# Kernel optimization log

Hardware: AMD Instinct MI355X
Metric: run time of the kernel (lower is better)

## Reference

```python
import jax, jax.numpy as jnp
import numpy as np

D_MODEL = 512
N_HEADS = 8
B, S = 4, 1024
REL_HIDDEN = 64


def setup_inputs() -> dict:
    key = jax.random.key(0)
    ks = jax.random.split(key, 16)

    def g(k, shape, scale=0.02):
        return jax.random.normal(k, shape, dtype=jnp.float32) * scale

    x = jax.random.normal(ks[0], (B, S, D_MODEL), dtype=jnp.float32)
    freqs = jax.random.uniform(ks[1], (B, S, 1), dtype=jnp.float32)
    return {
        "x": x,
        "freqs": freqs,
        "Wq": g(ks[2], (D_MODEL, D_MODEL)), "bq": g(ks[3], (D_MODEL,)),
        "Wk": g(ks[4], (D_MODEL, D_MODEL)), "bk": g(ks[5], (D_MODEL,)),
        "Wv": g(ks[6], (D_MODEL, D_MODEL)), "bv": g(ks[7], (D_MODEL,)),
        "Wo": g(ks[8], (D_MODEL, D_MODEL)), "bo": g(ks[9], (D_MODEL,)),
        "W1": g(ks[10], (2, REL_HIDDEN)), "b1": g(ks[11], (REL_HIDDEN,)),
        "W2": g(ks[12], (REL_HIDDEN, N_HEADS)), "b2": g(ks[13], (N_HEADS,)),
    }


def reference(x, freqs, Wq, bq, Wk, bk, Wv, bv, Wo, bo, W1, b1, W2, b2):
    b, s, d = x.shape
    h = N_HEADS
    dh = d // h

    def proj(W, bias):  # (b,s,d) -> (b,h,s,dh)
        return (x @ W + bias).reshape(b, s, h, dh).transpose(0, 2, 1, 3)

    Q = proj(Wq, bq)
    K = proj(Wk, bk)
    V = proj(Wv, bv)

    scores = jnp.einsum('bhid,bhjd->bhij', Q, K) / jnp.sqrt(jnp.float32(dh))

    # per-pair relative-frequency features: (b,s,s,2)
    eps = 1e-6
    fd = freqs[:, :, None, :] - freqs[:, None, :, :]
    fr = jnp.log((freqs[:, :, None, :] + eps) / (freqs[:, None, :, :] + eps))
    rel = jnp.concatenate([fd, fr], axis=-1)

    # MLP bias -> (b,s,s,h) -> (b,h,s,s)
    bias = jax.nn.relu(rel @ W1 + b1) @ W2 + b2
    scores = scores + jnp.transpose(bias, (0, 3, 1, 2))

    attn = jax.nn.softmax(scores, axis=-1)
    ctx = jnp.einsum('bhij,bhjd->bhid', attn, V)
    ctx = ctx.transpose(0, 2, 1, 3).reshape(b, s, d)
    return ctx @ Wo + bo
```

## Files before the change

kernel.cpp:

```cpp
#include <hip/hip_runtime.h>
#include <hip/hip_bf16.h>
#include <cstdint>

#define BATCH   4
#define SEQ     1024
#define DM      512
#define NH      8
#define DH      64
#define RH      64

typedef float f32x4 __attribute__((ext_vector_type(4)));
typedef __bf16 bf16x8 __attribute__((ext_vector_type(8)));

#define QB_OFF    (0)
#define KB_OFF    (4  << 20)
#define VT_OFF    (8  << 20)
#define XB_OFF    (12 << 20)
#define WT_OFF    (16 << 20)
#define WOT_OFF   (18 << 20)
#define AW_OFF    (20 << 20)
#define CW_OFF    (21 << 20)
#define CTXB_OFF  (22 << 20)
#define BIAS_OFF  (32 << 20)

__global__ __launch_bounds__(256) void cast_x(
    const float* __restrict__ x, __bf16* __restrict__ xb)
{
    const size_t i = ((size_t)blockIdx.x * 256 + threadIdx.x) * 8;
    const float4 a = *(const float4*)&x[i];
    const float4 b = *(const float4*)&x[i + 4];
    bf16x8 o;
    o[0] = (__bf16)a.x; o[1] = (__bf16)a.y; o[2] = (__bf16)a.z; o[3] = (__bf16)a.w;
    o[4] = (__bf16)b.x; o[5] = (__bf16)b.y; o[6] = (__bf16)b.z; o[7] = (__bf16)b.w;
    *(bf16x8*)&xb[i] = o;
}

__global__ __launch_bounds__(256) void cast_w(
    const float* __restrict__ Wq, const float* __restrict__ Wk,
    const float* __restrict__ Wv, const float* __restrict__ Wo,
    __bf16* __restrict__ Wt, __bf16* __restrict__ Wot)
{
    const int t = threadIdx.x;
    const int k0 = blockIdx.x * 64;
    const int n0 = blockIdx.y * 64;
    const int z  = blockIdx.z;
    const float* __restrict__ src = (z == 0) ? Wq : (z == 1) ? Wk : (z == 2) ? Wv : Wo;
    __bf16* __restrict__ dst = (z < 3) ? (Wt + (size_t)(z * 512 + n0) * 512)
                                       : (Wot + (size_t)n0 * 512);

    __shared__ __align__(16) float Ts[64][65];
    #pragma unroll
    for (int i = 0; i < 4; ++i) {
        const int id = t + i * 256;
        const int row = id >> 4, c4 = (id & 15) * 4;
        const float4 v = *(const float4*)&src[(size_t)(k0 + row) * DM + n0 + c4];
        Ts[row][c4 + 0] = v.x; Ts[row][c4 + 1] = v.y;
        Ts[row][c4 + 2] = v.z; Ts[row][c4 + 3] = v.w;
    }
    __syncthreads();
    #pragma unroll
    for (int i = 0; i < 2; ++i) {
        const int id = t + i * 256;
        const int rn = id >> 3, ck = (id & 7) * 8;
        bf16x8 o;
        #pragma unroll
        for (int j = 0; j < 8; ++j) o[j] = (__bf16)Ts[ck + j][rn];
        *(bf16x8*)&dst[(size_t)rn * 512 + k0 + ck] = o;
    }
}

__global__ __launch_bounds__(256) void gemm_qkv_mfma(
    const __bf16* __restrict__ xb, const __bf16* __restrict__ Wt,
    const float* __restrict__ bq, const float* __restrict__ bk,
    const float* __restrict__ bv,
    __bf16* __restrict__ Qb, __bf16* __restrict__ Kb, __bf16* __restrict__ Vtb)
{
    const int t = threadIdx.x;
    const int wave = t >> 6, lane = t & 63;
    const int wm = wave >> 1, wn = wave & 1;
    const int r = lane & 15, kc = lane >> 4, q4 = kc * 4;
    const int m0 = blockIdx.y * 128;
    const int n0 = blockIdx.x * 128;
    const int sec = n0 >> 9;
    const int nn = n0 & 511;

    __shared__ __align__(16) char smem[36864];
    __bf16* __restrict__ As = (__bf16*)smem;
    __bf16* __restrict__ Bs = (__bf16*)(smem + 18432);

    f32x4 acc[4][4];
    #pragma unroll
    for (int i = 0; i < 4; ++i)
        #pragma unroll
        for (int j = 0; j < 4; ++j) acc[i][j] = {0.f, 0.f, 0.f, 0.f};

    const int srow = t >> 3, sck = (t & 7) * 8;
    const __bf16* __restrict__ Ag = xb + (size_t)(m0 + srow) * 512 + sck;
    const __bf16* __restrict__ Bg = Wt + (size_t)(n0 + srow) * 512 + sck;

    for (int k0 = 0; k0 < 512; k0 += 64) {
        bf16x8 ra[4], rb[4];
        #pragma unroll
        for (int i = 0; i < 4; ++i) {
            ra[i] = *(const bf16x8*)(Ag + (size_t)i * 32 * 512 + k0);
            rb[i] = *(const bf16x8*)(Bg + (size_t)i * 32 * 512 + k0);
        }
        __syncthreads();
        #pragma unroll
        for (int i = 0; i < 4; ++i) {
            *(bf16x8*)&As[(srow + i * 32) * 72 + sck] = ra[i];
            *(bf16x8*)&Bs[(srow + i * 32) * 72 + sck] = rb[i];
        }
        __syncthreads();
        #pragma unroll
        for (int ks = 0; ks < 2; ++ks) {
            bf16x8 af[4], bf[4];
            #pragma unroll
            for (int mf = 0; mf < 4; ++mf)
                af[mf] = *(const bf16x8*)&As[(wm * 64 + mf * 16 + r) * 72 + ks * 32 + kc * 8];
            #pragma unroll
            for (int nf = 0; nf < 4; ++nf)
                bf[nf] = *(const bf16x8*)&Bs[(wn * 64 + nf * 16 + r) * 72 + ks * 32 + kc * 8];
            #pragma unroll
            for (int mf = 0; mf < 4; ++mf)
                #pragma unroll
                for (int nf = 0; nf < 4; ++nf)
                    acc[mf][nf] = __builtin_amdgcn_mfma_f32_16x16x32_bf16(
                        af[mf], bf[nf], acc[mf][nf], 0, 0, 0);
        }
    }

    const float* __restrict__ bias = (sec == 0) ? bq : (sec == 1) ? bk : bv;
    __syncthreads();
    __bf16* __restrict__ Ls = (__bf16*)smem;
    if (sec < 2) {
        #pragma unroll
        for (int mf = 0; mf < 4; ++mf)
            #pragma unroll
            for (int nf = 0; nf < 4; ++nf) {
                const int n_l = wn * 64 + nf * 16 + r;
                const float bb = bias[nn + n_l];
                #pragma unroll
                for (int rr = 0; rr < 4; ++rr)
                    Ls[(wm * 64 + mf * 16 + q4 + rr) * 136 + n_l] =
                        (__bf16)(acc[mf][nf][rr] + bb);
            }
    } else {
        #pragma unroll
        for (int mf = 0; mf < 4; ++mf)
            #pragma unroll
            for (int nf = 0; nf < 4; ++nf) {
                const int n_l = wn * 64 + nf * 16 + r;
                const float bb = bias[nn + n_l];
                #pragma unroll
                for (int rr = 0; rr < 4; ++rr)
                    Ls[n_l * 136 + (wm * 64 + mf * 16 + q4 + rr)] =
                        (__bf16)(acc[mf][nf][rr] + bb);
            }
    }
    __syncthreads();

    const int b = m0 >> 10, sbase = m0 & 1023;
    if (sec < 2) {
        __bf16* __restrict__ dst = sec ? Kb : Qb;
        #pragma unroll
        for (int i = 0; i < 8; ++i) {
            const int id = t + i * 256;
            const int row = id >> 4, nc = (id & 15) * 8;
            const bf16x8 v = *(const bf16x8*)&Ls[row * 136 + nc];
            const int ng = nn + nc, h = ng >> 6, c = ng & 63;
            *(bf16x8*)&dst[((size_t)(b * NH + h) * SEQ + sbase + row) * DH + c] = v;
        }
    } else {
        #pragma unroll
        for (int i = 0; i < 8; ++i) {
            const int id = t + i * 256;
            const int nrow = id >> 4, mc = (id & 15) * 8;
            const bf16x8 v = *(const bf16x8*)&Ls[nrow * 136 + mc];
            const int ng = nn + nrow, h = ng >> 6, c = ng & 63;
            *(bf16x8*)&Vtb[((size_t)(b * NH + h) * DH + c) * SEQ + sbase + mc] = v;
        }
    }
}

__global__ __launch_bounds__(256) void gemm_out_mfma(
    const __bf16* __restrict__ ctxb, const __bf16* __restrict__ Wot,
    const float* __restrict__ bo, float* __restrict__ out)
{
    const int t = threadIdx.x;
    const int wave = t >> 6, lane = t & 63;
    const int wm = wave >> 1, wn = wave & 1;
    const int r = lane & 15, kc = lane >> 4, q4 = kc * 4;
    const int m0 = blockIdx.y * 128;
    const int n0 = blockIdx.x * 128;

    __shared__ __align__(16) char smem[36864];
    __bf16* __restrict__ As = (__bf16*)smem;
    __bf16* __restrict__ Bs = (__bf16*)(smem + 18432);

    f32x4 acc[4][4];
    #pragma unroll
    for (int i = 0; i < 4; ++i)
        #pragma unroll
        for (int j = 0; j < 4; ++j) acc[i][j] = {0.f, 0.f, 0.f, 0.f};

    const int srow = t >> 3, sck = (t & 7) * 8;
    const __bf16* __restrict__ Ag = ctxb + (size_t)(m0 + srow) * 512 + sck;
    const __bf16* __restrict__ Bg = Wot + (size_t)(n0 + srow) * 512 + sck;

    for (int k0 = 0; k0 < 512; k0 += 64) {
        bf16x8 ra[4], rb[4];
        #pragma unroll
        for (int i = 0; i < 4; ++i) {
            ra[i] = *(const bf16x8*)(Ag + (size_t)i * 32 * 512 + k0);
            rb[i] = *(const bf16x8*)(Bg + (size_t)i * 32 * 512 + k0);
        }
        __syncthreads();
        #pragma unroll
        for (int i = 0; i < 4; ++i) {
            *(bf16x8*)&As[(srow + i * 32) * 72 + sck] = ra[i];
            *(bf16x8*)&Bs[(srow + i * 32) * 72 + sck] = rb[i];
        }
        __syncthreads();
        #pragma unroll
        for (int ks = 0; ks < 2; ++ks) {
            bf16x8 af[4], bf[4];
            #pragma unroll
            for (int mf = 0; mf < 4; ++mf)
                af[mf] = *(const bf16x8*)&As[(wm * 64 + mf * 16 + r) * 72 + ks * 32 + kc * 8];
            #pragma unroll
            for (int nf = 0; nf < 4; ++nf)
                bf[nf] = *(const bf16x8*)&Bs[(wn * 64 + nf * 16 + r) * 72 + ks * 32 + kc * 8];
            #pragma unroll
            for (int mf = 0; mf < 4; ++mf)
                #pragma unroll
                for (int nf = 0; nf < 4; ++nf)
                    acc[mf][nf] = __builtin_amdgcn_mfma_f32_16x16x32_bf16(
                        af[mf], bf[nf], acc[mf][nf], 0, 0, 0);
        }
    }

    #pragma unroll
    for (int mf = 0; mf < 4; ++mf)
        #pragma unroll
        for (int nf = 0; nf < 4; ++nf) {
            const int n_l = wn * 64 + nf * 16 + r;
            const float bb = bo[n0 + n_l];
            #pragma unroll
            for (int rr = 0; rr < 4; ++rr)
                out[(size_t)(m0 + wm * 64 + mf * 16 + q4 + rr) * DM + n0 + n_l] =
                    acc[mf][nf][rr] + bb;
        }
}

__global__ __launch_bounds__(64) void rel_kernel(
    const float* __restrict__ freqs,
    const float* __restrict__ W1,
    const float* __restrict__ b1,
    float* __restrict__ Aw,
    float* __restrict__ Cw)
{
    const int row = blockIdx.x;
    const int k = threadIdx.x;
    const float f = freqs[row];
    const float L = logf(f + 1e-6f);
    const float base = f * W1[k] + L * W1[RH + k];
    Aw[(size_t)row * RH + k] = base + b1[k];
    Cw[(size_t)row * RH + k] = -base;
}

__global__ __launch_bounds__(256) void bias_kernel(
    const float* __restrict__ Aw, const float* __restrict__ Cw,
    const float* __restrict__ W2, __bf16* __restrict__ biasb)
{
    const int t = threadIdx.x;
    const int j0 = blockIdx.x * 64;
    const int i0 = blockIdx.y * 16;
    const int b  = blockIdx.z;

    __shared__ __align__(16) float Ast[64][20];
    __shared__ __align__(16) float Cs[64][68];
    __shared__ __align__(16) float W2s[64][8];

    {
        const int rr = t >> 4, kq = (t & 15) * 4;
        float4 a4 = *(const float4*)&Aw[((size_t)b * SEQ + i0 + rr) * RH + kq];
        Ast[kq + 0][rr] = a4.x;
        Ast[kq + 1][rr] = a4.y;
        Ast[kq + 2][rr] = a4.z;
        Ast[kq + 3][rr] = a4.w;
        const int jr = t >> 2, kq2 = (t & 3) * 16;
        #pragma unroll
        for (int q = 0; q < 4; ++q) {
            float4 c4 = *(const float4*)&Cw[((size_t)b * SEQ + j0 + jr) * RH + kq2 + q * 4];
            Cs[kq2 + q * 4 + 0][jr] = c4.x;
            Cs[kq2 + q * 4 + 1][jr] = c4.y;
            Cs[kq2 + q * 4 + 2][jr] = c4.z;
            Cs[kq2 + q * 4 + 3][jr] = c4.w;
        }
        if (t < 64) {
            *(float4*)&W2s[t][0] = *(const float4*)&W2[t * 8 + 0];
            *(float4*)&W2s[t][4] = *(const float4*)&W2[t * 8 + 4];
        }
    }
    __syncthreads();

    const int jl = t & 63, ig = t >> 6;
    float acc[4][8];
    #pragma unroll
    for (int ii = 0; ii < 4; ++ii)
        #pragma unroll
        for (int hh = 0; hh < 8; ++hh) acc[ii][hh] = 0.f;

    #pragma unroll 4
    for (int k = 0; k < 64; ++k) {
        const float c  = Cs[k][jl];
        const float4 a4 = *(const float4*)&Ast[k][ig * 4];
        const float4 w0 = *(const float4*)&W2s[k][0];
        const float4 w1 = *(const float4*)&W2s[k][4];
        const float hv[4] = {
            fmaxf(a4.x + c, 0.f), fmaxf(a4.y + c, 0.f),
            fmaxf(a4.z + c, 0.f), fmaxf(a4.w + c, 0.f)};
        #pragma unroll
        for (int ii = 0; ii < 4; ++ii) {
            acc[ii][0] = fmaf(hv[ii], w0.x, acc[ii][0]);
            acc[ii][1] = fmaf(hv[ii], w0.y, acc[ii][1]);
            acc[ii][2] = fmaf(hv[ii], w0.z, acc[ii][2]);
            acc[ii][3] = fmaf(hv[ii], w0.w, acc[ii][3]);
            acc[ii][4] = fmaf(hv[ii], w1.x, acc[ii][4]);
            acc[ii][5] = fmaf(hv[ii], w1.y, acc[ii][5]);
            acc[ii][6] = fmaf(hv[ii], w1.z, acc[ii][6]);
            acc[ii][7] = fmaf(hv[ii], w1.w, acc[ii][7]);
        }
    }

    #pragma unroll
    for (int hh = 0; hh < 8; ++hh)
        #pragma unroll
        for (int ii = 0; ii < 4; ++ii)
            biasb[(((size_t)b * NH + hh) * SEQ + i0 + ig * 4 + ii) * SEQ + j0 + jl]
                = (__bf16)acc[ii][hh];
}

#define SSTR 1028
#define PSTR 1032

__global__ __launch_bounds__(512) void attn_mfma(
    const __bf16* __restrict__ Qb, const __bf16* __restrict__ Kb,
    const __bf16* __restrict__ Vtb, const __bf16* __restrict__ biasb,
    __bf16* __restrict__ ctxb)
{
    const int t = threadIdx.x;
    const int wave = t >> 6, lane = t & 63;
    const int r = lane & 15, kc = lane >> 4;
    const int blk = blockIdx.x;
    const int it = blk & 63;
    const int h  = (blk >> 6) & 7;
    const int b  = blk >> 9;
    const int s0 = it * 16;
    const int bh = b * NH + h;

    __shared__ __align__(16) float Ss[16 * SSTR];
    __shared__ float invl[16];

    {
        const __bf16* __restrict__ Qp = Qb + ((size_t)bh * SEQ + s0) * DH;
        const __bf16* __restrict__ Kp = Kb + (size_t)bh * SEQ * DH;
        const bf16x8 qa0 = *(const bf16x8*)(Qp + r * DH + kc * 8);
        const bf16x8 qa1 = *(const bf16x8*)(Qp + r * DH + 32 + kc * 8);
        #pragma unroll
        for (int jt = 0; jt < 8; ++jt) {
            const int j0 = wave * 128 + jt * 16;
            const bf16x8 kb0 = *(const bf16x8*)(Kp + (size_t)(j0 + r) * DH + kc * 8);
            const bf16x8 kb1 = *(const bf16x8*)(Kp + (size_t)(j0 + r) * DH + 32 + kc * 8);
            f32x4 acc = {0.f, 0.f, 0.f, 0.f};
            acc = __builtin_amdgcn_mfma_f32_16x16x32_bf16(qa0, kb0, acc, 0, 0, 0);
            acc = __builtin_amdgcn_mfma_f32_16x16x32_bf16(qa1, kb1, acc, 0, 0, 0);
            #pragma unroll
            for (int rr = 0; rr < 4; ++rr)
                Ss[(kc * 4 + rr) * SSTR + j0 + r] = acc[rr] * 0.125f;
        }
    }
    __syncthreads();

    {
        const int row = t >> 5, ln = t & 31;
        const __bf16* __restrict__ bp =
            biasb + ((size_t)bh * SEQ + (s0 + row)) * SEQ;
        float sv[32];
        float m = -1e30f;
        #pragma unroll
        for (int jj = 0; jj < 32; ++jj) {
            const float s = Ss[row * SSTR + jj * 32 + ln] + (float)bp[jj * 32 + ln];
            sv[jj] = s;
            m = fmaxf(m, s);
        }
        #pragma unroll
        for (int mask = 16; mask >= 1; mask >>= 1)
            m = fmaxf(m, __shfl_xor(m, mask));
        float l = 0.f;
        #pragma unroll
        for (int jj = 0; jj < 32; ++jj) {
            const float p = __expf(sv[jj] - m);
            sv[jj] = p;
            l += p;
        }
        #pragma unroll
        for (int mask = 16; mask >= 1; mask >>= 1)
            l += __shfl_xor(l, mask);
        if (ln == 0) invl[row] = 1.0f / l;
        __syncthreads();
        __bf16* __restrict__ Pb = (__bf16*)Ss;
        #pragma unroll
        for (int jj = 0; jj < 32; ++jj)
            Pb[row * PSTR + jj * 32 + ln] = (__bf16)sv[jj];
    }
    __syncthreads();

    {
        const int ct = wave & 3, kh = wave >> 2;
        const __bf16* __restrict__ Pb = (const __bf16*)Ss;
        const __bf16* __restrict__ Vp =
            Vtb + ((size_t)bh * DH + ct * 16 + r) * SEQ + kh * 512;
        f32x4 acc = {0.f, 0.f, 0.f, 0.f};
        #pragma unroll 4
        for (int jt = 0; jt < 16; ++jt) {
            const bf16x8 pa = *(const bf16x8*)(Pb + (size_t)r * PSTR + kh * 512 + jt * 32 + kc * 8);
            const bf16x8 vb = *(const bf16x8*)(Vp + jt * 32 + kc * 8);
            acc = __builtin_amdgcn_mfma_f32_16x16x32_bf16(pa, vb, acc, 0, 0, 0);
        }
        float* __restrict__ part = Ss + 8256;
        if (kh == 1) {
            #pragma unroll
            for (int rr = 0; rr < 4; ++rr)
                part[ct * 272 + (kc * 4 + rr) * 17 + r] = acc[rr];
        }
        __syncthreads();
        if (kh == 0) {
            #pragma unroll
            for (int rr = 0; rr < 4; ++rr) {
                const int row = kc * 4 + rr;
                const float v = (acc[rr] + part[ct * 272 + row * 17 + r]) * invl[row];
                ctxb[((size_t)(b * SEQ) + s0 + row) * DM + h * DH + ct * 16 + r] = (__bf16)v;
            }
        }
    }
}

extern "C" void kernel_launch(void* const* d_in, const int* in_sizes, int n_in,
                              void* d_out, int out_size, void* d_ws, size_t ws_size,
                              hipStream_t stream)
{
    const float* x     = (const float*)d_in[0];
    const float* freqs = (const float*)d_in[1];
    const float* Wq    = (const float*)d_in[2];
    const float* bq    = (const float*)d_in[3];
    const float* Wk    = (const float*)d_in[4];
    const float* bk    = (const float*)d_in[5];
    const float* Wv    = (const float*)d_in[6];
    const float* bv    = (const float*)d_in[7];
    const float* Wo    = (const float*)d_in[8];
    const float* bo    = (const float*)d_in[9];
    const float* W1    = (const float*)d_in[10];
    const float* b1    = (const float*)d_in[11];
    const float* W2    = (const float*)d_in[12];

    char* wsb = (char*)d_ws;
    __bf16* Qb    = (__bf16*)(wsb + QB_OFF);
    __bf16* Kb    = (__bf16*)(wsb + KB_OFF);
    __bf16* Vtb   = (__bf16*)(wsb + VT_OFF);
    __bf16* xb    = (__bf16*)(wsb + XB_OFF);
    __bf16* Wt    = (__bf16*)(wsb + WT_OFF);
    __bf16* Wot   = (__bf16*)(wsb + WOT_OFF);
    float*  Aw    = (float*)(wsb + AW_OFF);
    float*  Cw    = (float*)(wsb + CW_OFF);
    __bf16* ctxb  = (__bf16*)(wsb + CTXB_OFF);
    __bf16* biasb = (__bf16*)(wsb + BIAS_OFF);
    float* out = (float*)d_out;

    cast_x<<<dim3(1024), 256, 0, stream>>>(x, xb);
    cast_w<<<dim3(8, 8, 4), 256, 0, stream>>>(Wq, Wk, Wv, Wo, Wt, Wot);
    gemm_qkv_mfma<<<dim3(12, 32), 256, 0, stream>>>(xb, Wt, bq, bk, bv, Qb, Kb, Vtb);
    rel_kernel<<<dim3(4096), 64, 0, stream>>>(freqs, W1, b1, Aw, Cw);
    bias_kernel<<<dim3(16, 64, 4), 256, 0, stream>>>(Aw, Cw, W2, biasb);
    attn_mfma<<<dim3(2048), 512, 0, stream>>>(Qb, Kb, Vtb, biasb, ctxb);
    gemm_out_mfma<<<dim3(4, 32), 256, 0, stream>>>(ctxb, Wot, bo, out);
}
```

Baseline: 239.8 us.

## Compute relative-position bias MLP with MFMA and vectorize attention bias loads

Replaces the scalar-FMA bias kernel with an MFMA version: the ReLU hidden activations are built per pair in bf16 and multiplied by a bf16, zero-padded transposed W2 using 16x16x32 MFMA, with larger j tiles per block. The attention kernel now prefetches its bias row with 16-byte vector loads before the QK^T stage, vectorizes the softmax reads and P stores, and raises wave priority around the MFMA loops. This targets the FP32 ALU cost of the per-pair MLP and the scattered 2-byte bias loads, at the cost of rounding hidden activations to bf16 and wasting half the MFMA output rows on padding heads.

```diff
diff --git a/kernel.cpp b/kernel.cpp
--- a/kernel.cpp
+++ b/kernel.cpp
@@ -18,6 +18,7 @@
 #define XB_OFF    (12 << 20)
 #define WT_OFF    (16 << 20)
 #define WOT_OFF   (18 << 20)
+#define W2T_OFF   (19 << 20)
 #define AW_OFF    (20 << 20)
 #define CW_OFF    (21 << 20)
 #define CTXB_OFF  (22 << 20)
@@ -66,6 +67,18 @@
         #pragma unroll
         for (int j = 0; j < 8; ++j) o[j] = (__bf16)Ts[ck + j][rn];
         *(bf16x8*)&dst[(size_t)rn * 512 + k0 + ck] = o;
+    }
+}
+
+__global__ __launch_bounds__(256) void w2t_kernel(
+    const float* __restrict__ W2, __bf16* __restrict__ W2t)
+{
+    const int t = threadIdx.x;
+    #pragma unroll
+    for (int r = 0; r < 4; ++r) {
+        const int id = t + r * 256;
+        const int h = id >> 6, k = id & 63;
+        W2t[id] = (h < NH) ? (__bf16)W2[k * NH + h] : (__bf16)0.f;
     }
 }
 
@@ -269,77 +282,83 @@
     Cw[(size_t)row * RH + k] = -base;
 }
 
-__global__ __launch_bounds__(256) void bias_kernel(
+__global__ __launch_bounds__(256) void bias_mfma(
     const float* __restrict__ Aw, const float* __restrict__ Cw,
-    const float* __restrict__ W2, __bf16* __restrict__ biasb)
+    const __bf16* __restrict__ W2t, __bf16* __restrict__ biasb)
 {
     const int t = threadIdx.x;
-    const int j0 = blockIdx.x * 64;
+    const int wave = t >> 6, lane = t & 63;
+    const int jl = lane & 15, kc = lane >> 4;
+    const int j0 = blockIdx.x * 128;
     const int i0 = blockIdx.y * 16;
     const int b  = blockIdx.z;
 
-    __shared__ __align__(16) float Ast[64][20];
-    __shared__ __align__(16) float Cs[64][68];
-    __shared__ __align__(16) float W2s[64][8];
+    __shared__ __align__(16) float Cs[128][68];
 
     {
-        const int rr = t >> 4, kq = (t & 15) * 4;
-        float4 a4 = *(const float4*)&Aw[((size_t)b * SEQ + i0 + rr) * RH + kq];
-        Ast[kq + 0][rr] = a4.x;
-        Ast[kq + 1][rr] = a4.y;
-        Ast[kq + 2][rr] = a4.z;
-        Ast[kq + 3][rr] = a4.w;
-        const int jr = t >> 2, kq2 = (t & 3) * 16;
-        #pragma unroll
-        for (int q = 0; q < 4; ++q) {
-            float4 c4 = *(const float4*)&Cw[((size_t)b * SEQ + j0 + jr) * RH + kq2 + q * 4];
-            Cs[kq2 + q * 4 + 0][jr] = c4.x;
-            Cs[kq2 + q * 4 + 1][jr] = c4.y;
-            Cs[kq2 + q * 4 + 2][jr] = c4.z;
-            Cs[kq2 + q * 4 + 3][jr] = c4.w;
-        }
-        if (t < 64) {
-            *(float4*)&W2s[t][0] = *(const float4*)&W2[t * 8 + 0];
-            *(float4*)&W2s[t][4] = *(const float4*)&W2[t * 8 + 4];
-        }
-    }
+        const int jr = t >> 1, half = (t & 1) * 32;
+        const float* __restrict__ src = &Cw[((size_t)b * SEQ + j0 + jr) * RH + half];
+        #pragma unroll
+        for (int q = 0; q < 8; ++q) {
+            const float4 v = *(const float4*)(src + q * 4);
+            *(float4*)&Cs[jr][half + q * 4] = v;
+        }
+    }
+
+    const bf16x8 w2f0 = *(const bf16x8*)&W2t[jl * 64 + kc * 8];
+    const bf16x8 w2f1 = *(const bf16x8*)&W2t[jl * 64 + 32 + kc * 8];
+
     __syncthreads();
 
-    const int jl = t & 63, ig = t >> 6;
-    float acc[4][8];
-    #pragma unroll
-    for (int ii = 0; ii < 4; ++ii)
-        #pragma unroll
-        for (int hh = 0; hh < 8; ++hh) acc[ii][hh] = 0.f;
-
-    #pragma unroll 4
-    for (int k = 0; k < 64; ++k) {
-        const float c  = Cs[k][jl];
-        const float4 a4 = *(const float4*)&Ast[k][ig * 4];
-        const float4 w0 = *(const float4*)&W2s[k][0];
-        const float4 w1 = *(const float4*)&W2s[k][4];
-        const float hv[4] = {
-            fmaxf(a4.x + c, 0.f), fmaxf(a4.y + c, 0.f),
-            fmaxf(a4.z + c, 0.f), fmaxf(a4.w + c, 0.f)};
-        #pragma unroll
-        for (int ii = 0; ii < 4; ++ii) {
-            acc[ii][0] = fmaf(hv[ii], w0.x, acc[ii][0]);
-            acc[ii][1] = fmaf(hv[ii], w0.y, acc[ii][1]);
-            acc[ii][2] = fmaf(hv[ii], w0.z, acc[ii][2]);
-            acc[ii][3] = fmaf(hv[ii], w0.w, acc[ii][3]);
-            acc[ii][4] = fmaf(hv[ii], w1.x, acc[ii][4]);
-            acc[ii][5] = fmaf(hv[ii], w1.y, acc[ii][5]);
-            acc[ii][6] = fmaf(hv[ii], w1.z, acc[ii][6]);
-            acc[ii][7] = fmaf(hv[ii], w1.w, acc[ii][7]);
-        }
-    }
-
-    #pragma unroll
-    for (int hh = 0; hh < 8; ++hh)
-        #pragma unroll
-        for (int ii = 0; ii < 4; ++ii)
-            biasb[(((size_t)b * NH + hh) * SEQ + i0 + ig * 4 + ii) * SEQ + j0 + jl]
-                = (__bf16)acc[ii][hh];
+    const int iw = i0 + wave * 4;
+    #pragma unroll
+    for (int ii = 0; ii < 4; ++ii) {
+        const int i = iw + ii;
+        const float* __restrict__ ap = &Aw[((size_t)b * SEQ + i) * RH];
+        const float4 a0 = *(const float4*)(ap + kc * 8);
+        const float4 a1 = *(const float4*)(ap + kc * 8 + 4);
+        const float4 a2 = *(const float4*)(ap + 32 + kc * 8);
+        const float4 a3 = *(const float4*)(ap + 32 + kc * 8 + 4);
+
+        #pragma unroll
+        for (int jt = 0; jt < 8; ++jt) {
+            const float* __restrict__ cp = &Cs[jt * 16 + jl][kc * 8];
+            f32x4 acc = {0.f, 0.f, 0.f, 0.f};
+
+            const float4 c0 = *(const float4*)(cp);
+            const float4 c1 = *(const float4*)(cp + 4);
+            bf16x8 hb0;
+            hb0[0] = (__bf16)fmaxf(a0.x + c0.x, 0.f);
+            hb0[1] = (__bf16)fmaxf(a0.y + c0.y, 0.f);
+            hb0[2] = (__bf16)fmaxf(a0.z + c0.z, 0.f);
+            hb0[3] = (__bf16)fmaxf(a0.w + c0.w, 0.f);
+            hb0[4] = (__bf16)fmaxf(a1.x + c1.x, 0.f);
+            hb0[5] = (__bf16)fmaxf(a1.y + c1.y, 0.f);
+            hb0[6] = (__bf16)fmaxf(a1.z + c1.z, 0.f);
+            hb0[7] = (__bf16)fmaxf(a1.w + c1.w, 0.f);
+            acc = __builtin_amdgcn_mfma_f32_16x16x32_bf16(w2f0, hb0, acc, 0, 0, 0);
+
+            const float4 c2 = *(const float4*)(cp + 32);
+            const float4 c3 = *(const float4*)(cp + 36);
+            bf16x8 hb1;
+            hb1[0] = (__bf16)fmaxf(a2.x + c2.x, 0.f);
+            hb1[1] = (__bf16)fmaxf(a2.y + c2.y, 0.f);
+            hb1[2] = (__bf16)fmaxf(a2.z + c2.z, 0.f);
+            hb1[3] = (__bf16)fmaxf(a2.w + c2.w, 0.f);
+            hb1[4] = (__bf16)fmaxf(a3.x + c3.x, 0.f);
+            hb1[5] = (__bf16)fmaxf(a3.y + c3.y, 0.f);
+            hb1[6] = (__bf16)fmaxf(a3.z + c3.z, 0.f);
+            hb1[7] = (__bf16)fmaxf(a3.w + c3.w, 0.f);
+            acc = __builtin_amdgcn_mfma_f32_16x16x32_bf16(w2f1, hb1, acc, 0, 0, 0);
+
+            if (kc < 2) {
+                #pragma unroll
+                for (int rr = 0; rr < 4; ++rr)
+                    biasb[(((size_t)b * NH + kc * 4 + rr) * SEQ + i) * SEQ
+                          + j0 + jt * 16 + jl] = (__bf16)acc[rr];
+            }
+        }
+    }
 }
 
 #define SSTR 1028
@@ -363,11 +382,20 @@
     __shared__ __align__(16) float Ss[16 * SSTR];
     __shared__ float invl[16];
 
+    const int prow = t >> 5, pln = t & 31;
+    const __bf16* __restrict__ bpre =
+        biasb + ((size_t)bh * SEQ + s0 + prow) * SEQ + pln * 8;
+    const bf16x8 bre0 = *(const bf16x8*)(bpre);
+    const bf16x8 bre1 = *(const bf16x8*)(bpre + 256);
+    const bf16x8 bre2 = *(const bf16x8*)(bpre + 512);
+    const bf16x8 bre3 = *(const bf16x8*)(bpre + 768);
+
     {
         const __bf16* __restrict__ Qp = Qb + ((size_t)bh * SEQ + s0) * DH;
         const __bf16* __restrict__ Kp = Kb + (size_t)bh * SEQ * DH;
         const bf16x8 qa0 = *(const bf16x8*)(Qp + r * DH + kc * 8);
         const bf16x8 qa1 = *(const bf16x8*)(Qp + r * DH + 32 + kc * 8);
+        __builtin_amdgcn_s_setprio(1);
         #pragma unroll
         for (int jt = 0; jt < 8; ++jt) {
             const int j0 = wave * 128 + jt * 16;
@@ -380,20 +408,28 @@
             for (int rr = 0; rr < 4; ++rr)
                 Ss[(kc * 4 + rr) * SSTR + j0 + r] = acc[rr] * 0.125f;
         }
+        __builtin_amdgcn_s_setprio(0);
     }
     __syncthreads();
 
     {
-        const int row = t >> 5, ln = t & 31;
-        const __bf16* __restrict__ bp =
-            biasb + ((size_t)bh * SEQ + (s0 + row)) * SEQ;
+        const float* __restrict__ sp = &Ss[prow * SSTR + pln * 8];
         float sv[32];
         float m = -1e30f;
         #pragma unroll
-        for (int jj = 0; jj < 32; ++jj) {
-            const float s = Ss[row * SSTR + jj * 32 + ln] + (float)bp[jj * 32 + ln];
-            sv[jj] = s;
-            m = fmaxf(m, s);
+        for (int c = 0; c < 4; ++c) {
+            const float4 sa = *(const float4*)(sp + c * 256);
+            const float4 sb = *(const float4*)(sp + c * 256 + 4);
+            const bf16x8 br = (c == 0) ? bre0 : (c == 1) ? bre1 : (c == 2) ? bre2 : bre3;
+            float s;
+            s = sa.x + (float)br[0]; sv[c * 8 + 0] = s; m = fmaxf(m, s);
+            s = sa.y + (float)br[1]; sv[c * 8 + 1] = s; m = fmaxf(m, s);
+            s = sa.z + (float)br[2]; sv[c * 8 + 2] = s; m = fmaxf(m, s);
+            s = sa.w + (float)br[3]; sv[c * 8 + 3] = s; m = fmaxf(m, s);
+            s = sb.x + (float)br[4]; sv[c * 8 + 4] = s; m = fmaxf(m, s);
+            s = sb.y + (float)br[5]; sv[c * 8 + 5] = s; m = fmaxf(m, s);
+            s = sb.z + (float)br[6]; sv[c * 8 + 6] = s; m = fmaxf(m, s);
+            s = sb.w + (float)br[7]; sv[c * 8 + 7] = s; m = fmaxf(m, s);
         }
         #pragma unroll
         for (int mask = 16; mask >= 1; mask >>= 1)
@@ -408,12 +444,16 @@
         #pragma unroll
         for (int mask = 16; mask >= 1; mask >>= 1)
             l += __shfl_xor(l, mask);
-        if (ln == 0) invl[row] = 1.0f / l;
+        if (pln == 0) invl[prow] = 1.0f / l;
         __syncthreads();
         __bf16* __restrict__ Pb = (__bf16*)Ss;
         #pragma unroll
-        for (int jj = 0; jj < 32; ++jj)
-            Pb[row * PSTR + jj * 32 + ln] = (__bf16)sv[jj];
+        for (int c = 0; c < 4; ++c) {
+            bf16x8 pv;
+            #pragma unroll
+            for (int e = 0; e < 8; ++e) pv[e] = (__bf16)sv[c * 8 + e];
+            *(bf16x8*)&Pb[prow * PSTR + c * 256 + pln * 8] = pv;
+        }
     }
     __syncthreads();
 
@@ -423,12 +463,14 @@
         const __bf16* __restrict__ Vp =
             Vtb + ((size_t)bh * DH + ct * 16 + r) * SEQ + kh * 512;
         f32x4 acc = {0.f, 0.f, 0.f, 0.f};
+        __builtin_amdgcn_s_setprio(1);
         #pragma unroll 4
         for (int jt = 0; jt < 16; ++jt) {
             const bf16x8 pa = *(const bf16x8*)(Pb + (size_t)r * PSTR + kh * 512 + jt * 32 + kc * 8);
             const bf16x8 vb = *(const bf16x8*)(Vp + jt * 32 + kc * 8);
             acc = __builtin_amdgcn_mfma_f32_16x16x32_bf16(pa, vb, acc, 0, 0, 0);
         }
+        __builtin_amdgcn_s_setprio(0);
         float* __restrict__ part = Ss + 8256;
         if (kh == 1) {
             #pragma unroll
@@ -472,6 +514,7 @@
     __bf16* xb    = (__bf16*)(wsb + XB_OFF);
     __bf16* Wt    = (__bf16*)(wsb + WT_OFF);
     __bf16* Wot   = (__bf16*)(wsb + WOT_OFF);
+    __bf16* W2t   = (__bf16*)(wsb + W2T_OFF);
     float*  Aw    = (float*)(wsb + AW_OFF);
     float*  Cw    = (float*)(wsb + CW_OFF);
     __bf16* ctxb  = (__bf16*)(wsb + CTXB_OFF);
@@ -480,9 +523,10 @@
 
     cast_x<<<dim3(1024), 256, 0, stream>>>(x, xb);
     cast_w<<<dim3(8, 8, 4), 256, 0, stream>>>(Wq, Wk, Wv, Wo, Wt, Wot);
+    w2t_kernel<<<dim3(1), 256, 0, stream>>>(W2, W2t);
+    rel_kernel<<<dim3(4096), 64, 0, stream>>>(freqs, W1, b1, Aw, Cw);
     gemm_qkv_mfma<<<dim3(12, 32), 256, 0, stream>>>(xb, Wt, bq, bk, bv, Qb, Kb, Vtb);
-    rel_kernel<<<dim3(4096), 64, 0, stream>>>(freqs, W1, b1, Aw, Cw);
-    bias_kernel<<<dim3(16, 64, 4), 256, 0, stream>>>(Aw, Cw, W2, biasb);
+    bias_mfma<<<dim3(8, 64, 4), 256, 0, stream>>>(Aw, Cw, W2t, biasb);
     attn_mfma<<<dim3(2048), 512, 0, stream>>>(Qb, Kb, Vtb, biasb, ctxb);
     gemm_out_mfma<<<dim3(4, 32), 256, 0, stream>>>(ctxb, Wot, bo, out);
 }
```

New measurement: 221.8 us. -7.5%, faster.
